# Kernel tuning notes

Hardware: AMD Instinct MI355X
Metric: run time of the kernel (lower is better)

Reference implementation:

```python
import jax, jax.numpy as jnp
import numpy as np

B, L, D, H = 2, 2048, 1024, 16
HD = D // H
SCALE = HD ** -0.5


def setup_inputs() -> dict:
    key = jax.random.key(0)
    ks = jax.random.split(key, 11)
    s = D ** -0.5  # torch Linear default init scale (uniform bound)
    return {
        "q": jax.random.normal(ks[0], (B, L, D), jnp.float32),
        "k": jax.random.normal(ks[1], (B, L, D), jnp.float32),
        "v": jax.random.normal(ks[2], (B, L, D), jnp.float32),
        "Wq": jax.random.uniform(ks[3], (D, D), jnp.float32, -s, s),
        "bq": jax.random.uniform(ks[4], (D,), jnp.float32, -s, s),
        "Wk": jax.random.uniform(ks[5], (D, D), jnp.float32, -s, s),
        "bk": jax.random.uniform(ks[6], (D,), jnp.float32, -s, s),
        "Wv": jax.random.uniform(ks[7], (D, D), jnp.float32, -s, s),
        "bv": jax.random.uniform(ks[8], (D,), jnp.float32, -s, s),
        "Wo": jax.random.uniform(ks[9], (D, D), jnp.float32, -s, s),
        "bo": jax.random.uniform(ks[10], (D,), jnp.float32, -s, s),
    }


def reference(q, k, v, Wq, bq, Wk, bk, Wv, bv, Wo, bo):
    b, q_len, _ = q.shape
    # projections; weights stored as (D, D) acting on the right: x @ W + b
    qh = (q @ Wq + bq).reshape(b, q_len, H, HD).transpose(0, 2, 1, 3)  # (B,H,Q,hd)
    kh = (k @ Wk + bk).reshape(b, -1, H, HD).transpose(0, 2, 1, 3)    # (B,H,K,hd)
    vh = (v @ Wv + bv).reshape(b, -1, H, HD).transpose(0, 2, 1, 3)    # (B,H,K,hd)
    att = jnp.einsum("bhqd,bhkd->bhqk", qh * SCALE, kh)               # (B,H,Q,K)
    att = jax.nn.softmax(att, axis=-1)
    out = jnp.einsum("bhqk,bhkd->bhqd", att, vh)                      # (B,H,Q,hd)
    out = out.transpose(0, 2, 1, 3).reshape(b, q_len, D)
    return out @ Wo + bo
```

## Files before the change

kernel.cpp:

```cpp
#include <hip/hip_runtime.h>

namespace {
constexpr int kB  = 2;
constexpr int kL  = 2048;
constexpr int kD  = 1024;
constexpr int kH  = 16;
constexpr int kHD = 64;
constexpr int kM  = kB * kL;
}

typedef _Float16 f16x8 __attribute__((ext_vector_type(8)));
typedef float    f32x16 __attribute__((ext_vector_type(16)));
typedef unsigned int u32;

union Frag16 { uint4 u4; unsigned u[4]; f16x8 v; };

__device__ __forceinline__ unsigned short f2h(float f) {
    return __builtin_bit_cast(unsigned short, (_Float16)f);
}
__device__ __forceinline__ unsigned pk2(float a, float b) {
    return __builtin_bit_cast(unsigned, __builtin_amdgcn_cvt_pkrtz(a, b));
}

__device__ __forceinline__ void gload16(const void* g, void* l) {
    __builtin_amdgcn_global_load_lds(
        (const __attribute__((address_space(1))) u32*)g,
        (__attribute__((address_space(3))) u32*)(unsigned long long)(__builtin_bit_cast(unsigned long long, l)),
        16, 0, 0);
}

__global__ __launch_bounds__(256) void cast_f16_kernel(
    const float* __restrict__ q, const float* __restrict__ k,
    const float* __restrict__ v, unsigned short* __restrict__ dst)
{
    const float* src = blockIdx.y == 0 ? q : (blockIdx.y == 1 ? k : v);
    unsigned short* d = dst + (size_t)blockIdx.y * ((size_t)kM * kD);
    const size_t i = ((size_t)blockIdx.x * 256 + threadIdx.x) * 8;
    const float4 f0 = *(const float4*)(src + i);
    const float4 f1 = *(const float4*)(src + i + 4);
    _Float16 h[8];
    h[0] = (_Float16)f0.x; h[1] = (_Float16)f0.y;
    h[2] = (_Float16)f0.z; h[3] = (_Float16)f0.w;
    h[4] = (_Float16)f1.x; h[5] = (_Float16)f1.y;
    h[6] = (_Float16)f1.z; h[7] = (_Float16)f1.w;
    *(uint4*)(d + i) = *(uint4*)h;
}

__global__ __launch_bounds__(256) void tcast_kernel(
    const float* __restrict__ W0, const float* __restrict__ W1,
    const float* __restrict__ W2, const float* __restrict__ W3,
    unsigned short* __restrict__ WtBase)
{
    __shared__ _Float16 T[64][68];
    const float* W = blockIdx.z == 0 ? W0 : blockIdx.z == 1 ? W1
                   : blockIdx.z == 2 ? W2 : W3;
    unsigned short* Wt = WtBase + (size_t)blockIdx.z * ((size_t)kD * kD);
    const int k0 = blockIdx.y * 64, n0 = blockIdx.x * 64;
    const int tx = threadIdx.x & 15, ty = threadIdx.x >> 4;
#pragma unroll
    for (int i = 0; i < 4; ++i) {
        const int kk = i * 16 + ty;
        const float4 w = *(const float4*)&W[(size_t)(k0 + kk) * kD + n0 + tx * 4];
        T[tx * 4 + 0][kk] = (_Float16)w.x;
        T[tx * 4 + 1][kk] = (_Float16)w.y;
        T[tx * 4 + 2][kk] = (_Float16)w.z;
        T[tx * 4 + 3][kk] = (_Float16)w.w;
    }
    __syncthreads();
#pragma unroll
    for (int i = 0; i < 4; ++i) {
        const int nn = i * 16 + ty;
        *(ushort4*)&Wt[(size_t)(n0 + nn) * kD + k0 + tx * 4] = *(ushort4*)&T[nn][tx * 4];
    }
}

template <int MODE>
__global__ __launch_bounds__(256) void gemm16_kernel(
    const unsigned short* __restrict__ A, const unsigned short* __restrict__ Wt,
    const float* __restrict__ bias, void* __restrict__ Cv)
{
    __shared__ unsigned short Als[2][128 * 64];
    __shared__ unsigned short Bls[2][128 * 64];

    const int tid = threadIdx.x;
    const int lane = tid & 63;
    const int wid = tid >> 6;
    const int l31 = lane & 31;
    const int hi = lane >> 5;
    const int by = blockIdx.x & 31;
    const int bx = blockIdx.x >> 5;
    const int row0 = by * 128;
    const int col0 = bx * 128;
    const int wr = wid >> 1, wc = wid & 1;

    const int rl = lane >> 3;
    const int sl = lane & 7;
    const int ssrc = (sl ^ rl) * 8;

    const unsigned short* Abase = A + (size_t)(row0 + wid * 32 + rl) * kD + ssrc;
    const unsigned short* Bbase = Wt + (size_t)(col0 + wid * 32 + rl) * kD + ssrc;

    f32x16 acc00{}, acc01{}, acc10{}, acc11{};

    auto stage = [&](int kt, int buf) {
#pragma unroll
        for (int i = 0; i < 4; ++i) {
            gload16(Abase + (size_t)(i * 8) * kD + kt * 64,
                    &Als[buf][(wid * 32 + i * 8) * 64]);
        }
#pragma unroll
        for (int i = 0; i < 4; ++i) {
            gload16(Bbase + (size_t)(i * 8) * kD + kt * 64,
                    &Bls[buf][(wid * 32 + i * 8) * 64]);
        }
    };

    const int ra0 = wr * 64 + l31;
    const int cb0 = wc * 64 + l31;

    stage(0, 0);
    int cur = 0;
    for (int kt = 0; kt < kD / 64; ++kt) {
        __syncthreads();
        if (kt + 1 < kD / 64) stage(kt + 1, cur ^ 1);
#pragma unroll
        for (int ks = 0; ks < 4; ++ks) {
            const int slot = (ks << 1) | hi;
            Frag16 a0, a1, b0, b1;
            a0.u4 = *(const uint4*)&Als[cur][ra0 * 64 + ((slot ^ (ra0 & 7)) << 3)];
            a1.u4 = *(const uint4*)&Als[cur][(ra0 + 32) * 64 + ((slot ^ ((ra0 + 32) & 7)) << 3)];
            b0.u4 = *(const uint4*)&Bls[cur][cb0 * 64 + ((slot ^ (cb0 & 7)) << 3)];
            b1.u4 = *(const uint4*)&Bls[cur][(cb0 + 32) * 64 + ((slot ^ ((cb0 + 32) & 7)) << 3)];
            acc00 = __builtin_amdgcn_mfma_f32_32x32x16_f16(a0.v, b0.v, acc00, 0, 0, 0);
            acc01 = __builtin_amdgcn_mfma_f32_32x32x16_f16(a0.v, b1.v, acc01, 0, 0, 0);
            acc10 = __builtin_amdgcn_mfma_f32_32x32x16_f16(a1.v, b0.v, acc10, 0, 0, 0);
            acc11 = __builtin_amdgcn_mfma_f32_32x32x16_f16(a1.v, b1.v, acc11, 0, 0, 0);
        }
        cur ^= 1;
    }

    const float bias0 = bias[col0 + wc * 64 + l31];
    const float bias1 = bias[col0 + wc * 64 + 32 + l31];

    const f32x16* accs[2][2] = {{&acc00, &acc01}, {&acc10, &acc11}};
#pragma unroll
    for (int rt = 0; rt < 2; ++rt) {
#pragma unroll
        for (int ct = 0; ct < 2; ++ct) {
            const f32x16& acv = *accs[rt][ct];
            const float bb = ct ? bias1 : bias0;
            const int c = col0 + wc * 64 + ct * 32 + l31;
            if (MODE == 2) {
                unsigned short* C = (unsigned short*)Cv;
#pragma unroll
                for (int qd = 0; qd < 4; ++qd) {
                    const int r = row0 + wr * 64 + rt * 32 + 8 * qd + 4 * hi;
                    const int b_ = r >> 11, l_ = r & (kL - 1);
                    ushort4 w;
                    w.x = f2h(acv[4 * qd + 0] + bb);
                    w.y = f2h(acv[4 * qd + 1] + bb);
                    w.z = f2h(acv[4 * qd + 2] + bb);
                    w.w = f2h(acv[4 * qd + 3] + bb);
                    *(ushort4*)&C[((size_t)(b_ * kH + (c >> 6)) * kHD + (c & 63)) * kL + l_] = w;
                }
            } else {
#pragma unroll
                for (int reg = 0; reg < 16; ++reg) {
                    const int r = row0 + wr * 64 + rt * 32 + (reg & 3) + 8 * (reg >> 2) + 4 * hi;
                    const float val = acv[reg] + bb;
                    if (MODE == 0) {
                        ((float*)Cv)[(size_t)r * kD + c] = val;
                    } else {
                        const int b_ = r >> 11, l_ = r & (kL - 1);
                        ((unsigned short*)Cv)[((size_t)(b_ * kH + (c >> 6)) * kL + l_) * kHD + (c & 63)] = f2h(val);
                    }
                }
            }
        }
    }
}

__global__ __launch_bounds__(512) void attn_mfma_kernel(
    const unsigned short* __restrict__ Qh, const unsigned short* __restrict__ Kh,
    const unsigned short* __restrict__ Vt, unsigned short* __restrict__ Opart,
    float2* __restrict__ Stat)
{
    __shared__ unsigned short Kls[2][64 * 64];
    __shared__ unsigned short Vls[2][64 * 64];

    const int lane = threadIdx.x & 63;
    const int wid  = threadIdx.x >> 6;
    const int l31  = lane & 31;
    const int hi   = lane >> 5;

    const int id = blockIdx.x;
    const int j  = id >> 3;
    const int bh = (id & 7) * 4 + (j >> 4);
    const int qt = j & 7;
    const int ks = (j >> 3) & 1;
    const int q = qt * 256 + wid * 32 + l31;

    const size_t qkBase = (size_t)bh * kL * kHD;
    const unsigned short* Qp = Qh + qkBase + (size_t)q * kHD + hi * 8;
    Frag16 qf[4];
#pragma unroll
    for (int d = 0; d < 4; ++d) qf[d].u4 = *(const uint4*)(Qp + d * 16);

    const int srow = wid * 8 + (lane >> 3);
    const int soff = (((lane & 7) ^ (srow & 7)) << 3);
    const unsigned short* Kg = Kh + qkBase + (size_t)srow * kHD + soff;
    const unsigned short* Vg = Vt + (size_t)bh * kHD * kL + (size_t)srow * kL + soff;

    auto stage = [&](int kt, int buf) {
        gload16(Kg + (size_t)(kt * 64) * kHD, &Kls[buf][(wid * 8) * 64]);
        gload16(Vg + kt * 64,                 &Vls[buf][(wid * 8) * 64]);
    };

    f32x16 o0{}, o1{};
    float m = -1e30f, lsum = 0.f;
    const float cexp = 0.125f * 1.44269504089f;

    const int kt0 = ks * 16;
    stage(kt0, 0);
    int cur = 0;
    for (int lt = 0; lt < 16; ++lt) {
        __syncthreads();
        if (lt + 1 < 16) stage(kt0 + lt + 1, cur ^ 1);

        const int rA = l31, rB = l31 + 32;
        f32x16 c0{}, c1{};
        Frag16 kf0[4], kf1[4];
#pragma unroll
        for (int d = 0; d < 4; ++d) {
            const int s = (d << 1) | hi;
            kf0[d].u4 = *(const uint4*)&Kls[cur][rA * 64 + ((s ^ (rA & 7)) << 3)];
            kf1[d].u4 = *(const uint4*)&Kls[cur][rB * 64 + ((s ^ (rB & 7)) << 3)];
        }
        Frag16 vf0[4], vf1[4];
#pragma unroll
        for (int ksl = 0; ksl < 4; ++ksl) {
            const int s = (ksl << 1) | hi;
            vf0[ksl].u4 = *(const uint4*)&Vls[cur][rA * 64 + ((s ^ (rA & 7)) << 3)];
            vf1[ksl].u4 = *(const uint4*)&Vls[cur][rB * 64 + ((s ^ (rB & 7)) << 3)];
        }
        __builtin_amdgcn_s_setprio(1);
#pragma unroll
        for (int d = 0; d < 4; ++d) {
            c0 = __builtin_amdgcn_mfma_f32_32x32x16_f16(kf0[d].v, qf[d].v, c0, 0, 0, 0);
            c1 = __builtin_amdgcn_mfma_f32_32x32x16_f16(kf1[d].v, qf[d].v, c1, 0, 0, 0);
        }
        __builtin_amdgcn_s_setprio(0);

        float mx = fmaxf(c0[0], c1[0]);
#pragma unroll
        for (int r = 1; r < 16; ++r) mx = fmaxf(mx, fmaxf(c0[r], c1[r]));
        mx = fmaxf(mx, __shfl_xor(mx, 32));
        if (mx > m + 48.f) {
            const float corr = __builtin_amdgcn_exp2f((m - mx) * cexp);
            m = mx;
            lsum *= corr;
            o0 *= corr;
            o1 *= corr;
        }
        const float mc = m * cexp;
        float p0[16], p1[16];
        float rs = 0.f;
#pragma unroll
        for (int r = 0; r < 16; ++r) {
            p0[r] = __builtin_amdgcn_exp2f(fmaf(c0[r], cexp, -mc));
            p1[r] = __builtin_amdgcn_exp2f(fmaf(c1[r], cexp, -mc));
            rs += p0[r] + p1[r];
        }
        rs += __shfl_xor(rs, 32);
        lsum += rs;

        unsigned u0[8], u1[8];
#pragma unroll
        for (int i = 0; i < 8; ++i) {
            u0[i] = pk2(p0[2 * i], p0[2 * i + 1]);
            u1[i] = pk2(p1[2 * i], p1[2 * i + 1]);
        }
        Frag16 pf[4];
        {
            unsigned t0 = hi ? u0[0] : u0[2];
            unsigned t1 = hi ? u0[1] : u0[3];
            unsigned t2 = hi ? u0[4] : u0[6];
            unsigned t3 = hi ? u0[5] : u0[7];
            const unsigned r0 = __shfl_xor(t0, 32);
            const unsigned r1 = __shfl_xor(t1, 32);
            const unsigned r2 = __shfl_xor(t2, 32);
            const unsigned r3 = __shfl_xor(t3, 32);
            pf[0].u[0] = hi ? r0 : u0[0];
            pf[0].u[1] = hi ? r1 : u0[1];
            pf[0].u[2] = hi ? u0[2] : r0;
            pf[0].u[3] = hi ? u0[3] : r1;
            pf[1].u[0] = hi ? r2 : u0[4];
            pf[1].u[1] = hi ? r3 : u0[5];
            pf[1].u[2] = hi ? u0[6] : r2;
            pf[1].u[3] = hi ? u0[7] : r3;
        }
        {
            unsigned t0 = hi ? u1[0] : u1[2];
            unsigned t1 = hi ? u1[1] : u1[3];
            unsigned t2 = hi ? u1[4] : u1[6];
            unsigned t3 = hi ? u1[5] : u1[7];
            const unsigned r0 = __shfl_xor(t0, 32);
            const unsigned r1 = __shfl_xor(t1, 32);
            const unsigned r2 = __shfl_xor(t2, 32);
            const unsigned r3 = __shfl_xor(t3, 32);
            pf[2].u[0] = hi ? r0 : u1[0];
            pf[2].u[1] = hi ? r1 : u1[1];
            pf[2].u[2] = hi ? u1[2] : r0;
            pf[2].u[3] = hi ? u1[3] : r1;
            pf[3].u[0] = hi ? r2 : u1[4];
            pf[3].u[1] = hi ? r3 : u1[5];
            pf[3].u[2] = hi ? u1[6] : r2;
            pf[3].u[3] = hi ? u1[7] : r3;
        }

        __builtin_amdgcn_s_setprio(1);
#pragma unroll
        for (int ksl = 0; ksl < 4; ++ksl) {
            o0 = __builtin_amdgcn_mfma_f32_32x32x16_f16(vf0[ksl].v, pf[ksl].v, o0, 0, 0, 0);
            o1 = __builtin_amdgcn_mfma_f32_32x32x16_f16(vf1[ksl].v, pf[ksl].v, o1, 0, 0, 0);
        }
        __builtin_amdgcn_s_setprio(0);
        cur ^= 1;
    }

    const size_t prow = (size_t)ks * (32 * kL) + (size_t)bh * kL + q;
    const float inv = 1.f / lsum;
    unsigned short* pp = Opart + prow * kHD;
#pragma unroll
    for (int g = 0; g < 4; ++g) {
        const int d = g * 8 + hi * 4;
        uint2 w0, w1;
        w0.x = pk2(o0[4 * g + 0] * inv, o0[4 * g + 1] * inv);
        w0.y = pk2(o0[4 * g + 2] * inv, o0[4 * g + 3] * inv);
        w1.x = pk2(o1[4 * g + 0] * inv, o1[4 * g + 1] * inv);
        w1.y = pk2(o1[4 * g + 2] * inv, o1[4 * g + 3] * inv);
        *(uint2*)(pp + d) = w0;
        *(uint2*)(pp + 32 + d) = w1;
    }
    if (hi == 0) Stat[prow] = make_float2(m, lsum);
}

__global__ __launch_bounds__(256) void merge_kernel(
    const unsigned short* __restrict__ Opart, const float2* __restrict__ Stat,
    unsigned short* __restrict__ O16)
{
    const int g = blockIdx.x * 256 + threadIdx.x;
    const int row = g >> 3;
    const int d0 = (g & 7) * 8;
    const int bh = row >> 11, q = row & (kL - 1);
    const float2 sa = Stat[row];
    const float2 sb = Stat[32 * kL + row];
    const float cexp = 0.125f * 1.44269504089f;
    const float M = fmaxf(sa.x, sb.x);
    float wa = __builtin_amdgcn_exp2f((sa.x - M) * cexp) * sa.y;
    float wb = __builtin_amdgcn_exp2f((sb.x - M) * cexp) * sb.y;
    const float inv = 1.f / (wa + wb);
    wa *= inv; wb *= inv;

    const unsigned short* pa = Opart + (size_t)row * kHD + d0;
    const unsigned short* pb = pa + (size_t)32 * kL * kHD;
    uint4 ua = *(const uint4*)pa;
    uint4 ub = *(const uint4*)pb;
    _Float16 ha[8], hb[8];
    *(uint4*)ha = ua;
    *(uint4*)hb = ub;
    unsigned out[4];
#pragma unroll
    for (int i = 0; i < 4; ++i) {
        const float v0 = wa * (float)ha[2 * i]     + wb * (float)hb[2 * i];
        const float v1 = wa * (float)ha[2 * i + 1] + wb * (float)hb[2 * i + 1];
        out[i] = pk2(v0, v1);
    }
    const int b_ = bh >> 4, h_ = bh & 15;
    *(uint4*)&O16[((size_t)(b_ * kL + q)) * kD + h_ * kHD + d0] = *(uint4*)out;
}

extern "C" void kernel_launch(void* const* d_in, const int* in_sizes, int n_in,
                              void* d_out, int out_size, void* d_ws, size_t ws_size,
                              hipStream_t stream)
{
    const float* q  = (const float*)d_in[0];
    const float* k  = (const float*)d_in[1];
    const float* v  = (const float*)d_in[2];
    const float* Wq = (const float*)d_in[3];
    const float* bq = (const float*)d_in[4];
    const float* Wk = (const float*)d_in[5];
    const float* bk = (const float*)d_in[6];
    const float* Wv = (const float*)d_in[7];
    const float* bv = (const float*)d_in[8];
    const float* Wo = (const float*)d_in[9];
    const float* bo = (const float*)d_in[10];
    float* out = (float*)d_out;

    const size_t MD = (size_t)kM * kD;
    const size_t DD = (size_t)kD * kD;
    unsigned short* A16 = (unsigned short*)d_ws;
    unsigned short* Wt16 = A16 + 3 * MD;
    unsigned short* Qh16 = Wt16 + 4 * DD;
    unsigned short* Kh16 = Qh16 + MD;
    unsigned short* Vt16 = Kh16 + MD;
    unsigned short* O16   = A16;
    unsigned short* Opart = A16 + MD;
    float2*         Stat  = (float2*)Wt16;

    const dim3 blk(256);

    hipLaunchKernelGGL(cast_f16_kernel, dim3(kM * kD / (256 * 8), 3), blk, 0, stream,
                       q, k, v, A16);
    hipLaunchKernelGGL(tcast_kernel, dim3(16, 16, 4), blk, 0, stream,
                       Wq, Wk, Wv, Wo, Wt16);

    hipLaunchKernelGGL((gemm16_kernel<1>), dim3(256), blk, 0, stream,
                       A16, Wt16, bq, (void*)Qh16);
    hipLaunchKernelGGL((gemm16_kernel<1>), dim3(256), blk, 0, stream,
                       A16 + MD, Wt16 + DD, bk, (void*)Kh16);
    hipLaunchKernelGGL((gemm16_kernel<2>), dim3(256), blk, 0, stream,
                       A16 + 2 * MD, Wt16 + 2 * DD, bv, (void*)Vt16);

    hipLaunchKernelGGL(attn_mfma_kernel, dim3(512), dim3(512), 0, stream,
                       Qh16, Kh16, Vt16, Opart, Stat);
    hipLaunchKernelGGL(merge_kernel, dim3(2048), blk, 0, stream,
                       Opart, Stat, O16);

    hipLaunchKernelGGL((gemm16_kernel<0>), dim3(256), blk, 0, stream,
                       O16, Wt16 + 3 * DD, bo, (void*)out);
}
```

Baseline: 142.9 us.

## Deepen attention K/V pipeline and compute row sums via ones-MFMA

The attention kernel moves from a double-buffered to a four-buffer K/V ring with two tiles in flight. It replaces __syncthreads with explicit vmcnt waits plus s_barrier. The softmax row sum is now accumulated on the matrix cores by multiplying the packed probabilities with a ones vector, which removes the VALU reduction and cross-lane shuffle. The max reduction uses v_max3 and the launch bound requests four blocks per CU. The costs are doubled LDS use, an extra MFMA per k-slice, and row sums taken from fp16-rounded probabilities.

```diff
diff --git a/kernel.cpp b/kernel.cpp
--- a/kernel.cpp
+++ b/kernel.cpp
@@ -20,6 +20,11 @@
 }
 __device__ __forceinline__ unsigned pk2(float a, float b) {
     return __builtin_bit_cast(unsigned, __builtin_amdgcn_cvt_pkrtz(a, b));
+}
+__device__ __forceinline__ float max3f(float a, float b, float c) {
+    float d;
+    asm("v_max3_f32 %0, %1, %2, %3" : "=v"(d) : "v"(a), "v"(b), "v"(c));
+    return d;
 }
 
 __device__ __forceinline__ void gload16(const void* g, void* l) {
@@ -180,13 +185,13 @@
     }
 }
 
-__global__ __launch_bounds__(512) void attn_mfma_kernel(
+__global__ __launch_bounds__(512, 4) void attn_mfma_kernel(
     const unsigned short* __restrict__ Qh, const unsigned short* __restrict__ Kh,
     const unsigned short* __restrict__ Vt, unsigned short* __restrict__ Opart,
     float2* __restrict__ Stat)
 {
-    __shared__ unsigned short Kls[2][64 * 64];
-    __shared__ unsigned short Vls[2][64 * 64];
+    __shared__ unsigned short Kls[4][64 * 64];
+    __shared__ unsigned short Vls[4][64 * 64];
 
     const int lane = threadIdx.x & 63;
     const int wid  = threadIdx.x >> 6;
@@ -216,16 +221,24 @@
         gload16(Vg + kt * 64,                 &Vls[buf][(wid * 8) * 64]);
     };
 
-    f32x16 o0{}, o1{};
-    float m = -1e30f, lsum = 0.f;
+    f16x8 onesv;
+#pragma unroll
+    for (int i = 0; i < 8; ++i) onesv[i] = (_Float16)1.0f;
+
+    f32x16 o0{}, o1{}, ls{};
+    float m = -1e30f;
     const float cexp = 0.125f * 1.44269504089f;
 
     const int kt0 = ks * 16;
-    stage(kt0, 0);
-    int cur = 0;
+    stage(kt0 + 0, 0);
+    stage(kt0 + 1, 1);
+
     for (int lt = 0; lt < 16; ++lt) {
-        __syncthreads();
-        if (lt + 1 < 16) stage(kt0 + lt + 1, cur ^ 1);
+        if (lt < 15) asm volatile("s_waitcnt vmcnt(2)" ::: "memory");
+        else         asm volatile("s_waitcnt vmcnt(0)" ::: "memory");
+        __builtin_amdgcn_s_barrier();
+        if (lt + 2 < 16) stage(kt0 + lt + 2, (lt + 2) & 3);
+        const int cur = lt & 3;
 
         const int rA = l31, rB = l31 + 32;
         f32x16 c0{}, c1{};
@@ -253,32 +266,24 @@
 
         float mx = fmaxf(c0[0], c1[0]);
 #pragma unroll
-        for (int r = 1; r < 16; ++r) mx = fmaxf(mx, fmaxf(c0[r], c1[r]));
+        for (int r = 1; r < 16; ++r) mx = max3f(mx, c0[r], c1[r]);
         mx = fmaxf(mx, __shfl_xor(mx, 32));
         if (mx > m + 48.f) {
             const float corr = __builtin_amdgcn_exp2f((m - mx) * cexp);
             m = mx;
-            lsum *= corr;
             o0 *= corr;
             o1 *= corr;
+            ls *= corr;
         }
         const float mc = m * cexp;
-        float p0[16], p1[16];
-        float rs = 0.f;
-#pragma unroll
-        for (int r = 0; r < 16; ++r) {
-            p0[r] = __builtin_amdgcn_exp2f(fmaf(c0[r], cexp, -mc));
-            p1[r] = __builtin_amdgcn_exp2f(fmaf(c1[r], cexp, -mc));
-            rs += p0[r] + p1[r];
-        }
-        rs += __shfl_xor(rs, 32);
-        lsum += rs;
 
         unsigned u0[8], u1[8];
 #pragma unroll
         for (int i = 0; i < 8; ++i) {
-            u0[i] = pk2(p0[2 * i], p0[2 * i + 1]);
-            u1[i] = pk2(p1[2 * i], p1[2 * i + 1]);
+            u0[i] = pk2(__builtin_amdgcn_exp2f(fmaf(c0[2 * i], cexp, -mc)),
+                        __builtin_amdgcn_exp2f(fmaf(c0[2 * i + 1], cexp, -mc)));
+            u1[i] = pk2(__builtin_amdgcn_exp2f(fmaf(c1[2 * i], cexp, -mc)),
+                        __builtin_amdgcn_exp2f(fmaf(c1[2 * i + 1], cexp, -mc)));
         }
         Frag16 pf[4];
         {
@@ -323,11 +328,12 @@
         for (int ksl = 0; ksl < 4; ++ksl) {
             o0 = __builtin_amdgcn_mfma_f32_32x32x16_f16(vf0[ksl].v, pf[ksl].v, o0, 0, 0, 0);
             o1 = __builtin_amdgcn_mfma_f32_32x32x16_f16(vf1[ksl].v, pf[ksl].v, o1, 0, 0, 0);
+            ls = __builtin_amdgcn_mfma_f32_32x32x16_f16(onesv, pf[ksl].v, ls, 0, 0, 0);
         }
         __builtin_amdgcn_s_setprio(0);
-        cur ^= 1;
-    }
-
+    }
+
+    const float lsum = ls[0];
     const size_t prow = (size_t)ks * (32 * kL) + (size_t)bh * kL + q;
     const float inv = 1.f / lsum;
     unsigned short* pp = Opart + prow * kHD;
```

New measurement: 246.8 us. 1.73x slower.
